# Performance work log

Measured on AMD Instinct MI355X. Metric: run time of the kernel, lower is better.

Reference implementation:

```python
import jax, jax.numpy as jnp
import numpy as np

N = 100_000      # nodes
E = 1_600_000    # edges (avg degree 16)
EP = 500_000     # pos/neg decode edges each
IN, H, OUT = 256, 128, 64


def setup_inputs() -> dict:
    key = jax.random.key(0)
    ks = jax.random.split(key, 8)
    x = jax.random.normal(ks[0], (N, IN), dtype=jnp.float32)
    edge_index = jax.random.randint(ks[1], (2, E), 0, N, dtype=jnp.int32)
    pos_edge_index = jax.random.randint(ks[2], (2, EP), 0, N, dtype=jnp.int32)
    neg_edge_index = jax.random.randint(ks[3], (2, EP), 0, N, dtype=jnp.int32)
    W1 = jax.random.normal(ks[4], (IN, H), dtype=jnp.float32) * (1.0 / np.sqrt(IN))
    b1 = jnp.zeros((H,), dtype=jnp.float32)
    W2 = jax.random.normal(ks[5], (H, OUT), dtype=jnp.float32) * (1.0 / np.sqrt(H))
    b2 = jnp.zeros((OUT,), dtype=jnp.float32)
    return dict(x=x, edge_index=edge_index, pos_edge_index=pos_edge_index,
                neg_edge_index=neg_edge_index, W1=W1, b1=b1, W2=W2, b2=b2)


def _gcn_conv(x, src, dst, norm, W, b, n_nodes):
    # PyG GCNConv: linear transform, then normalized scatter-add aggregation
    h = x @ W                              # [N, out]
    msg = h[src] * norm[:, None]           # gather + scale, [E+N, out]
    agg = jax.ops.segment_sum(msg, dst, num_segments=n_nodes)
    return agg + b


def reference(x, edge_index, pos_edge_index, neg_edge_index, W1, b1, W2, b2):
    n = x.shape[0]
    loops = jnp.arange(n, dtype=edge_index.dtype)
    src = jnp.concatenate([edge_index[0], loops])   # add self-loops (GCNConv default)
    dst = jnp.concatenate([edge_index[1], loops])
    # symmetric normalization D^{-1/2} (A+I) D^{-1/2}
    deg = jax.ops.segment_sum(jnp.ones_like(src, dtype=x.dtype), dst, num_segments=n)
    dinv = jnp.where(deg > 0, jax.lax.rsqrt(jnp.maximum(deg, 1e-12)), 0.0)
    norm = dinv[src] * dinv[dst]
    # encode
    h = jax.nn.relu(_gcn_conv(x, src, dst, norm, W1, b1, n))
    z = _gcn_conv(h, src, dst, norm, W2, b2, n)
    # decode: edge score = <z_u, z_v> over pos+neg edges
    ei = jnp.concatenate([pos_edge_index, neg_edge_index], axis=-1)
    return (z[ei[0]] * z[ei[1]]).sum(axis=-1)   # [2*EP]
```

## Files before the change

kernel.cpp:

```cpp
#include <hip/hip_runtime.h>


typedef __attribute__((ext_vector_type(8))) short short8;
typedef __attribute__((ext_vector_type(4))) float f32x4;

#define BUK_SHIFT 7
#define BUK_NODES 128

__global__ __launch_bounds__(256) void b_hist_k(const int* __restrict__ dst, int E,
                                                int nbuk, int* __restrict__ bhist) {
  __shared__ int h[1024];
  for (int i = threadIdx.x; i < nbuk; i += 256) h[i] = 0;
  __syncthreads();
  for (int i = blockIdx.x * 256 + threadIdx.x; i < E; i += gridDim.x * 256)
    atomicAdd(&h[dst[i] >> BUK_SHIFT], 1);
  __syncthreads();
  for (int i = threadIdx.x; i < nbuk; i += 256) {
    int c = h[i];
    if (c) atomicAdd(&bhist[i], c);
  }
}

__global__ __launch_bounds__(256) void b_scan_k(const int* __restrict__ bhist,
                                                int nbuk, int* __restrict__ bbase,
                                                int* __restrict__ bcur) {
  __shared__ int arr[256];
  const int t = threadIdx.x;
  const int per = (nbuk + 255) / 256;
  const int start = t * per;
  const int end = min(start + per, nbuk);
  int s = 0;
  for (int i = start; i < end; ++i) s += bhist[i];
  arr[t] = s;
  __syncthreads();
  for (int off = 1; off < 256; off <<= 1) {
    int v = (t >= off) ? arr[t - off] : 0;
    __syncthreads();
    arr[t] += v;
    __syncthreads();
  }
  int run = arr[t] - s;
  for (int i = start; i < end; ++i) {
    bbase[i] = run;
    bcur[i] = run;
    run += bhist[i];
  }
  if (t == 255) bbase[nbuk] = arr[255];
}

__global__ __launch_bounds__(256) void b_scatter_k(const int* __restrict__ src,
                                                   const int* __restrict__ dst, int E,
                                                   int nbuk, int* __restrict__ bcur,
                                                   int* __restrict__ ebuf) {
  __shared__ int lh[1024];
  __shared__ int lc[1024];
  const int base = blockIdx.x * 8192;
  if (base >= E) return;
  const int end = min(base + 8192, E);
  for (int i = threadIdx.x; i < nbuk; i += 256) lh[i] = 0;
  __syncthreads();
  for (int i = base + threadIdx.x; i < end; i += 256)
    atomicAdd(&lh[dst[i] >> BUK_SHIFT], 1);
  __syncthreads();
  for (int i = threadIdx.x; i < nbuk; i += 256) {
    int c = lh[i];
    lc[i] = c ? atomicAdd(&bcur[i], c) : 0;
  }
  __syncthreads();
  for (int i = base + threadIdx.x; i < end; i += 256) {
    int d = dst[i];
    int pos = atomicAdd(&lc[d >> BUK_SHIFT], 1);
    ebuf[pos] = src[i] | ((d & (BUK_NODES - 1)) << 17);
  }
}

__global__ __launch_bounds__(128) void b_build_k(const int* __restrict__ ebuf,
                                                 const int* __restrict__ bbase, int n,
                                                 int nbuk, float* __restrict__ dinv,
                                                 int* __restrict__ rowptr,
                                                 int* __restrict__ csr) {
  __shared__ int cnt[BUK_NODES];
  __shared__ int pre[BUK_NODES];
  __shared__ int cur[BUK_NODES];
  const int b = blockIdx.x, t = threadIdx.x;
  cnt[t] = 0;
  __syncthreads();
  const int beg = bbase[b], end = bbase[b + 1];
  for (int i = beg + t; i < end; i += 128) atomicAdd(&cnt[ebuf[i] >> 17], 1);
  __syncthreads();
  const int c = cnt[t];
  pre[t] = c;
  __syncthreads();
  for (int off = 1; off < 128; off <<= 1) {
    int v = (t >= off) ? pre[t - off] : 0;
    __syncthreads();
    pre[t] += v;
    __syncthreads();
  }
  const int base = beg + pre[t] - c;
  cur[t] = base;
  const int node = (b << BUK_SHIFT) + t;
  if (node < n) {
    rowptr[node] = base;
    dinv[node] = rsqrtf((float)(c + 1));
  }
  if (b == 0 && t == 0) rowptr[n] = bbase[nbuk];
  __syncthreads();
  for (int i = beg + t; i < end; i += 128) {
    int e = ebuf[i];
    int pos = atomicAdd(&cur[e >> 17], 1);
    csr[pos] = e & 0x1FFFF;
  }
}

__global__ __launch_bounds__(256) void split_w_k(const float* __restrict__ W, int K,
                                                 int N,
                                                 unsigned short* __restrict__ hi,
                                                 unsigned short* __restrict__ lo) {
  const int idx = blockIdx.x * 256 + threadIdx.x;
  if (idx >= K * N) return;
  const int k = idx / N, c = idx - k * N;
  const float a = W[idx];
  const unsigned u = __float_as_uint(a);
  const unsigned short h = (unsigned short)(u >> 16);
  const float l = a - __uint_as_float(u & 0xFFFF0000u);
  const unsigned short lb = (unsigned short)(__float_as_uint(l) >> 16);
  hi[(size_t)c * K + k] = h;
  lo[(size_t)c * K + k] = lb;
}

template <int BN>
__global__ __launch_bounds__(256) void gemm_mfma(
    const float* __restrict__ A, const unsigned short* __restrict__ Bthi,
    const unsigned short* __restrict__ Btlo, float* __restrict__ C,
    const float* __restrict__ rowscale, int M, int K) {
  constexpr int BM = 64, BK = 32;
  constexpr int NT = BN / 16;
  constexpr int LD = 40;
  __shared__ unsigned short Ahi[BM * LD];
  __shared__ unsigned short Alo[BM * LD];
  __shared__ unsigned short Bhi[BN * LD];
  __shared__ unsigned short Blo[BN * LD];
  const int tid = threadIdx.x;
  const int lane = tid & 63;
  const int wave = tid >> 6;
  const int rowBase = blockIdx.x * BM;

  f32x4 acc[NT];
#pragma unroll
  for (int c = 0; c < NT; ++c) acc[c] = (f32x4){0.f, 0.f, 0.f, 0.f};

  const int sr = tid >> 2;
  const int sk = (tid & 3) * 8;
  const int arow = wave * 16 + (lane & 15);
  const int akb = (lane >> 4) * 8;

  for (int k0 = 0; k0 < K; k0 += BK) {
    {
      const int gr = rowBase + sr;
      float4 v0 = make_float4(0.f, 0.f, 0.f, 0.f);
      float4 v1 = make_float4(0.f, 0.f, 0.f, 0.f);
      if (gr < M) {
        const float* p = A + (size_t)gr * K + k0 + sk;
        v0 = *reinterpret_cast<const float4*>(p);
        v1 = *reinterpret_cast<const float4*>(p + 4);
      }
      const float vv[8] = {v0.x, v0.y, v0.z, v0.w, v1.x, v1.y, v1.z, v1.w};
      short8 hv, lv;
#pragma unroll
      for (int i = 0; i < 8; ++i) {
        const unsigned u = __float_as_uint(vv[i]);
        hv[i] = (short)(u >> 16);
        const float l = vv[i] - __uint_as_float(u & 0xFFFF0000u);
        lv[i] = (short)(__float_as_uint(l) >> 16);
      }
      *reinterpret_cast<short8*>(&Ahi[sr * LD + sk]) = hv;
      *reinterpret_cast<short8*>(&Alo[sr * LD + sk]) = lv;
    }
    for (int i = tid; i < BN * 2; i += 256) {
      const int col = i >> 1;
      const int kk = (i & 1) * 16;
      const size_t gofs = (size_t)col * K + k0 + kk;
      *reinterpret_cast<short8*>(&Bhi[col * LD + kk]) =
          *reinterpret_cast<const short8*>(&Bthi[gofs]);
      *reinterpret_cast<short8*>(&Bhi[col * LD + kk + 8]) =
          *reinterpret_cast<const short8*>(&Bthi[gofs + 8]);
      *reinterpret_cast<short8*>(&Blo[col * LD + kk]) =
          *reinterpret_cast<const short8*>(&Btlo[gofs]);
      *reinterpret_cast<short8*>(&Blo[col * LD + kk + 8]) =
          *reinterpret_cast<const short8*>(&Btlo[gofs + 8]);
    }
    __syncthreads();
    const short8 fa_hi = *reinterpret_cast<const short8*>(&Ahi[arow * LD + akb]);
    const short8 fa_lo = *reinterpret_cast<const short8*>(&Alo[arow * LD + akb]);
#pragma unroll
    for (int c = 0; c < NT; ++c) {
      const int bofs = (c * 16 + (lane & 15)) * LD + akb;
      const short8 fb_hi = *reinterpret_cast<const short8*>(&Bhi[bofs]);
      const short8 fb_lo = *reinterpret_cast<const short8*>(&Blo[bofs]);
      acc[c] = __builtin_amdgcn_mfma_f32_16x16x32_bf16(fa_hi, fb_hi, acc[c], 0, 0, 0);
      acc[c] = __builtin_amdgcn_mfma_f32_16x16x32_bf16(fa_lo, fb_hi, acc[c], 0, 0, 0);
      acc[c] = __builtin_amdgcn_mfma_f32_16x16x32_bf16(fa_hi, fb_lo, acc[c], 0, 0, 0);
    }
    __syncthreads();
  }
  const int crow = rowBase + wave * 16 + (lane >> 4) * 4;
  float sc[4];
#pragma unroll
  for (int j = 0; j < 4; ++j) sc[j] = (crow + j < M) ? rowscale[crow + j] : 0.f;
#pragma unroll
  for (int c = 0; c < NT; ++c) {
#pragma unroll
    for (int j = 0; j < 4; ++j) {
      const int gr = crow + j;
      if (gr < M) C[(size_t)gr * BN + c * 16 + (lane & 15)] = acc[c][j] * sc[j];
    }
  }
}

template <bool RELU>
__global__ __launch_bounds__(256) void agg128_k(const float* __restrict__ g,
                                                const int* __restrict__ rowptr,
                                                const int* __restrict__ csr,
                                                const float* __restrict__ dinv,
                                                const float* __restrict__ bias,
                                                float* __restrict__ hout, int n) {
  const int wid = (blockIdx.x * 256 + threadIdx.x) >> 6;
  if (wid >= n) return;
  const int lane = threadIdx.x & 63;
  const int half = lane >> 5;
  const size_t col = (size_t)(lane & 31) * 4;
  const float dd = dinv[wid];
  const int beg = rowptr[wid];
  const int end = rowptr[wid + 1];
  float4 acc = make_float4(0.f, 0.f, 0.f, 0.f);
  int e = beg;
  for (; e + 8 <= end; e += 8) {
    const int s0 = csr[e + 0 + half];
    const int s1 = csr[e + 2 + half];
    const int s2 = csr[e + 4 + half];
    const int s3 = csr[e + 6 + half];
    const float4 v0 = *reinterpret_cast<const float4*>(&g[(size_t)s0 * 128 + col]);
    const float4 v1 = *reinterpret_cast<const float4*>(&g[(size_t)s1 * 128 + col]);
    const float4 v2 = *reinterpret_cast<const float4*>(&g[(size_t)s2 * 128 + col]);
    const float4 v3 = *reinterpret_cast<const float4*>(&g[(size_t)s3 * 128 + col]);
    acc.x += (v0.x + v1.x) + (v2.x + v3.x);
    acc.y += (v0.y + v1.y) + (v2.y + v3.y);
    acc.z += (v0.z + v1.z) + (v2.z + v3.z);
    acc.w += (v0.w + v1.w) + (v2.w + v3.w);
  }
  for (; e + 2 <= end; e += 2) {
    const int s = csr[e + half];
    const float4 v = *reinterpret_cast<const float4*>(&g[(size_t)s * 128 + col]);
    acc.x += v.x;
    acc.y += v.y;
    acc.z += v.z;
    acc.w += v.w;
  }
  if (e < end && half == 0) {
    const int s = csr[e];
    const float4 v = *reinterpret_cast<const float4*>(&g[(size_t)s * 128 + col]);
    acc.x += v.x;
    acc.y += v.y;
    acc.z += v.z;
    acc.w += v.w;
  }
  acc.x += __shfl_xor(acc.x, 32);
  acc.y += __shfl_xor(acc.y, 32);
  acc.z += __shfl_xor(acc.z, 32);
  acc.w += __shfl_xor(acc.w, 32);
  if (half == 0) {
    const float4 sv = *reinterpret_cast<const float4*>(&g[(size_t)wid * 128 + col]);
    const float4 b = *reinterpret_cast<const float4*>(&bias[col]);
    float4 r;
    r.x = dd * (acc.x + sv.x) + b.x;
    r.y = dd * (acc.y + sv.y) + b.y;
    r.z = dd * (acc.z + sv.z) + b.z;
    r.w = dd * (acc.w + sv.w) + b.w;
    if (RELU) {
      r.x = fmaxf(r.x, 0.f);
      r.y = fmaxf(r.y, 0.f);
      r.z = fmaxf(r.z, 0.f);
      r.w = fmaxf(r.w, 0.f);
    }
    *reinterpret_cast<float4*>(&hout[(size_t)wid * 128 + col]) = r;
  }
}

__global__ __launch_bounds__(256) void agg64_k(const float* __restrict__ g,
                                               const int* __restrict__ rowptr,
                                               const int* __restrict__ csr,
                                               const float* __restrict__ dinv,
                                               const float* __restrict__ bias,
                                               float* __restrict__ hout, int n) {
  const int wid = (blockIdx.x * 256 + threadIdx.x) >> 6;
  if (wid >= n) return;
  const int lane = threadIdx.x & 63;
  const int quad = lane >> 4;
  const size_t col = (size_t)(lane & 15) * 4;
  const float dd = dinv[wid];
  const int beg = rowptr[wid];
  const int end = rowptr[wid + 1];
  float4 acc = make_float4(0.f, 0.f, 0.f, 0.f);
  int e = beg;
  for (; e + 16 <= end; e += 16) {
    const int s0 = csr[e + 0 + quad];
    const int s1 = csr[e + 4 + quad];
    const int s2 = csr[e + 8 + quad];
    const int s3 = csr[e + 12 + quad];
    const float4 v0 = *reinterpret_cast<const float4*>(&g[(size_t)s0 * 64 + col]);
    const float4 v1 = *reinterpret_cast<const float4*>(&g[(size_t)s1 * 64 + col]);
    const float4 v2 = *reinterpret_cast<const float4*>(&g[(size_t)s2 * 64 + col]);
    const float4 v3 = *reinterpret_cast<const float4*>(&g[(size_t)s3 * 64 + col]);
    acc.x += (v0.x + v1.x) + (v2.x + v3.x);
    acc.y += (v0.y + v1.y) + (v2.y + v3.y);
    acc.z += (v0.z + v1.z) + (v2.z + v3.z);
    acc.w += (v0.w + v1.w) + (v2.w + v3.w);
  }
  for (; e + 4 <= end; e += 4) {
    const int s = csr[e + quad];
    const float4 v = *reinterpret_cast<const float4*>(&g[(size_t)s * 64 + col]);
    acc.x += v.x;
    acc.y += v.y;
    acc.z += v.z;
    acc.w += v.w;
  }
  const int r = end - e;
  if (quad < r) {
    const int s = csr[e + quad];
    const float4 v = *reinterpret_cast<const float4*>(&g[(size_t)s * 64 + col]);
    acc.x += v.x;
    acc.y += v.y;
    acc.z += v.z;
    acc.w += v.w;
  }
  acc.x += __shfl_xor(acc.x, 16);
  acc.y += __shfl_xor(acc.y, 16);
  acc.z += __shfl_xor(acc.z, 16);
  acc.w += __shfl_xor(acc.w, 16);
  acc.x += __shfl_xor(acc.x, 32);
  acc.y += __shfl_xor(acc.y, 32);
  acc.z += __shfl_xor(acc.z, 32);
  acc.w += __shfl_xor(acc.w, 32);
  if (quad == 0) {
    const float4 sv = *reinterpret_cast<const float4*>(&g[(size_t)wid * 64 + col]);
    const float4 b = *reinterpret_cast<const float4*>(&bias[col]);
    float4 res;
    res.x = dd * (acc.x + sv.x) + b.x;
    res.y = dd * (acc.y + sv.y) + b.y;
    res.z = dd * (acc.z + sv.z) + b.z;
    res.w = dd * (acc.w + sv.w) + b.w;
    *reinterpret_cast<float4*>(&hout[(size_t)wid * 64 + col]) = res;
  }
}

__global__ __launch_bounds__(256) void decode_k(const int* __restrict__ pos,
                                                const int* __restrict__ neg,
                                                const float* __restrict__ z,
                                                float* __restrict__ out, int EP) {
  const long long t = (long long)blockIdx.x * 256 + threadIdx.x;
  const long long e = t >> 3;
  const int lane = (int)(t & 7);
  if (e >= 2LL * EP) return;
  int u, v;
  if (e < EP) {
    u = pos[e];
    v = pos[EP + e];
  } else {
    u = neg[e - EP];
    v = neg[EP + (e - EP)];
  }
  const float* zu = &z[(size_t)u * 64 + lane * 8];
  const float* zv = &z[(size_t)v * 64 + lane * 8];
  const float4 a0 = *reinterpret_cast<const float4*>(zu);
  const float4 a1 = *reinterpret_cast<const float4*>(zu + 4);
  const float4 b0 = *reinterpret_cast<const float4*>(zv);
  const float4 b1 = *reinterpret_cast<const float4*>(zv + 4);
  float p = a0.x * b0.x + a0.y * b0.y + a0.z * b0.z + a0.w * b0.w +
            a1.x * b1.x + a1.y * b1.y + a1.z * b1.z + a1.w * b1.w;
#pragma unroll
  for (int off = 4; off > 0; off >>= 1) p += __shfl_down(p, off, 8);
  if (lane == 0) out[e] = p;
}


extern "C" void kernel_launch(void* const* d_in, const int* in_sizes, int n_in,
                              void* d_out, int out_size, void* d_ws, size_t ws_size,
                              hipStream_t stream) {
  const float* x = (const float*)d_in[0];
  const int* ei = (const int*)d_in[1];
  const int* pos = (const int*)d_in[2];
  const int* neg = (const int*)d_in[3];
  const float* W1 = (const float*)d_in[4];
  const float* b1 = (const float*)d_in[5];
  const float* W2 = (const float*)d_in[6];
  const float* b2 = (const float*)d_in[7];
  float* out = (float*)d_out;

  const int H = in_sizes[5];
  const int IN = in_sizes[4] / H;
  const int OUT = in_sizes[7];
  const int N = in_sizes[0] / IN;
  const int E = in_sizes[1] / 2;
  const int EP = in_sizes[2] / 2;

  char* ws = (char*)d_ws;
  size_t off = 0;
  auto carve = [&](size_t bytes) -> char* {
    char* p = ws + off;
    off += (bytes + 255) & ~(size_t)255;
    return p;
  };
  const int NBUK = (N + BUK_NODES - 1) >> BUK_SHIFT;

  float* dinvb = (float*)carve((size_t)N * 4);
  int* rowptr = (int*)carve((size_t)(N + 1) * 4);
  int* bhist = (int*)carve((size_t)NBUK * 4);
  int* bbase = (int*)carve((size_t)(NBUK + 1) * 4);
  int* bcur = (int*)carve((size_t)NBUK * 4);
  int* ebuf = (int*)carve((size_t)E * 4);
  int* csr = (int*)carve((size_t)E * 4);
  float* bufA = (float*)carve((size_t)N * H * 4);
  float* bufB = (float*)carve((size_t)N * H * 4);
  unsigned short* w1hi = (unsigned short*)carve((size_t)IN * H * 2);
  unsigned short* w1lo = (unsigned short*)carve((size_t)IN * H * 2);
  unsigned short* w2hi = (unsigned short*)carve((size_t)H * OUT * 2);
  unsigned short* w2lo = (unsigned short*)carve((size_t)H * OUT * 2);
  (void)ws_size;

  const int* srcp = ei;
  const int* dstp = ei + E;

  split_w_k<<<(IN * H + 255) / 256, 256, 0, stream>>>(W1, IN, H, w1hi, w1lo);
  split_w_k<<<(H * OUT + 255) / 256, 256, 0, stream>>>(W2, H, OUT, w2hi, w2lo);

  hipMemsetAsync(bhist, 0, (size_t)NBUK * 4, stream);
  b_hist_k<<<512, 256, 0, stream>>>(dstp, E, NBUK, bhist);
  b_scan_k<<<1, 256, 0, stream>>>(bhist, NBUK, bbase, bcur);
  b_scatter_k<<<(E + 8191) / 8192, 256, 0, stream>>>(srcp, dstp, E, NBUK, bcur, ebuf);
  b_build_k<<<NBUK, 128, 0, stream>>>(ebuf, bbase, N, NBUK, dinvb, rowptr, csr);

  gemm_mfma<128><<<(N + 63) / 64, 256, 0, stream>>>(x, w1hi, w1lo, bufA, dinvb, N, IN);
  agg128_k<true><<<(N + 3) / 4, 256, 0, stream>>>(bufA, rowptr, csr, dinvb, b1,
                                                  bufB, N);
  gemm_mfma<64><<<(N + 63) / 64, 256, 0, stream>>>(bufB, w2hi, w2lo, bufA, dinvb, N, H);
  agg64_k<<<(N + 3) / 4, 256, 0, stream>>>(bufA, rowptr, csr, dinvb, b2, bufB, N);
  const long long threads = 2LL * EP * 8;
  decode_k<<<(int)((threads + 255) / 256), 256, 0, stream>>>(pos, neg, bufB, out, EP);
}
```

Measured before the change: 377.7 us.

## Fuse layer-1 aggregation with layer-2 GEMM via shared-memory bf16 split tiles

Layer-1 neighbor aggregation (with bias and ReLU) now writes each 16-node tile into shared memory as hi/lo bf16 splits. The same block then multiplies the tile by W2 with MFMA and scales by dinv. This removes the global write and re-read of the 128-wide hidden activation and one kernel launch. In exchange, W2 fragments are loaded from global per block, and each block does a small MFMA tail after a barrier.

Measured after the change: 376.7 us. About the same (-0.3%).

```diff
diff --git a/kernel.cpp b/kernel.cpp
--- a/kernel.cpp
+++ b/kernel.cpp
@@ -218,72 +218,115 @@
   }
 }
 
-template <bool RELU>
-__global__ __launch_bounds__(256) void agg128_k(const float* __restrict__ g,
-                                                const int* __restrict__ rowptr,
-                                                const int* __restrict__ csr,
-                                                const float* __restrict__ dinv,
-                                                const float* __restrict__ bias,
-                                                float* __restrict__ hout, int n) {
-  const int wid = (blockIdx.x * 256 + threadIdx.x) >> 6;
-  if (wid >= n) return;
-  const int lane = threadIdx.x & 63;
+__global__ __launch_bounds__(256) void agg128_gemm2_k(
+    const float* __restrict__ g1, const int* __restrict__ rowptr,
+    const int* __restrict__ csr, const float* __restrict__ dinv,
+    const float* __restrict__ bias, const unsigned short* __restrict__ W2thi,
+    const unsigned short* __restrict__ W2tlo, float* __restrict__ g2, int n) {
+  constexpr int LD2 = 136;
+  __shared__ unsigned short Hhi[16 * LD2];
+  __shared__ unsigned short Hlo[16 * LD2];
+  const int tid = threadIdx.x;
+  const int lane = tid & 63;
+  const int wave = tid >> 6;
   const int half = lane >> 5;
+  const int nb = blockIdx.x * 16;
+
   const size_t col = (size_t)(lane & 31) * 4;
-  const float dd = dinv[wid];
-  const int beg = rowptr[wid];
-  const int end = rowptr[wid + 1];
-  float4 acc = make_float4(0.f, 0.f, 0.f, 0.f);
-  int e = beg;
-  for (; e + 8 <= end; e += 8) {
-    const int s0 = csr[e + 0 + half];
-    const int s1 = csr[e + 2 + half];
-    const int s2 = csr[e + 4 + half];
-    const int s3 = csr[e + 6 + half];
-    const float4 v0 = *reinterpret_cast<const float4*>(&g[(size_t)s0 * 128 + col]);
-    const float4 v1 = *reinterpret_cast<const float4*>(&g[(size_t)s1 * 128 + col]);
-    const float4 v2 = *reinterpret_cast<const float4*>(&g[(size_t)s2 * 128 + col]);
-    const float4 v3 = *reinterpret_cast<const float4*>(&g[(size_t)s3 * 128 + col]);
-    acc.x += (v0.x + v1.x) + (v2.x + v3.x);
-    acc.y += (v0.y + v1.y) + (v2.y + v3.y);
-    acc.z += (v0.z + v1.z) + (v2.z + v3.z);
-    acc.w += (v0.w + v1.w) + (v2.w + v3.w);
-  }
-  for (; e + 2 <= end; e += 2) {
-    const int s = csr[e + half];
-    const float4 v = *reinterpret_cast<const float4*>(&g[(size_t)s * 128 + col]);
-    acc.x += v.x;
-    acc.y += v.y;
-    acc.z += v.z;
-    acc.w += v.w;
-  }
-  if (e < end && half == 0) {
-    const int s = csr[e];
-    const float4 v = *reinterpret_cast<const float4*>(&g[(size_t)s * 128 + col]);
-    acc.x += v.x;
-    acc.y += v.y;
-    acc.z += v.z;
-    acc.w += v.w;
-  }
-  acc.x += __shfl_xor(acc.x, 32);
-  acc.y += __shfl_xor(acc.y, 32);
-  acc.z += __shfl_xor(acc.z, 32);
-  acc.w += __shfl_xor(acc.w, 32);
-  if (half == 0) {
-    const float4 sv = *reinterpret_cast<const float4*>(&g[(size_t)wid * 128 + col]);
-    const float4 b = *reinterpret_cast<const float4*>(&bias[col]);
-    float4 r;
-    r.x = dd * (acc.x + sv.x) + b.x;
-    r.y = dd * (acc.y + sv.y) + b.y;
-    r.z = dd * (acc.z + sv.z) + b.z;
-    r.w = dd * (acc.w + sv.w) + b.w;
-    if (RELU) {
-      r.x = fmaxf(r.x, 0.f);
-      r.y = fmaxf(r.y, 0.f);
-      r.z = fmaxf(r.z, 0.f);
-      r.w = fmaxf(r.w, 0.f);
-    }
-    *reinterpret_cast<float4*>(&hout[(size_t)wid * 128 + col]) = r;
+#pragma unroll
+  for (int it = 0; it < 4; ++it) {
+    const int row = wave * 4 + it;
+    const int node = nb + row;
+    float4 r = make_float4(0.f, 0.f, 0.f, 0.f);
+    if (node < n) {
+      const float dd = dinv[node];
+      const int beg = rowptr[node];
+      const int end = rowptr[node + 1];
+      float4 acc = make_float4(0.f, 0.f, 0.f, 0.f);
+      int e = beg;
+      for (; e + 8 <= end; e += 8) {
+        const int s0 = csr[e + 0 + half];
+        const int s1 = csr[e + 2 + half];
+        const int s2 = csr[e + 4 + half];
+        const int s3 = csr[e + 6 + half];
+        const float4 v0 = *reinterpret_cast<const float4*>(&g1[(size_t)s0 * 128 + col]);
+        const float4 v1 = *reinterpret_cast<const float4*>(&g1[(size_t)s1 * 128 + col]);
+        const float4 v2 = *reinterpret_cast<const float4*>(&g1[(size_t)s2 * 128 + col]);
+        const float4 v3 = *reinterpret_cast<const float4*>(&g1[(size_t)s3 * 128 + col]);
+        acc.x += (v0.x + v1.x) + (v2.x + v3.x);
+        acc.y += (v0.y + v1.y) + (v2.y + v3.y);
+        acc.z += (v0.z + v1.z) + (v2.z + v3.z);
+        acc.w += (v0.w + v1.w) + (v2.w + v3.w);
+      }
+      for (; e + 2 <= end; e += 2) {
+        const int s = csr[e + half];
+        const float4 v = *reinterpret_cast<const float4*>(&g1[(size_t)s * 128 + col]);
+        acc.x += v.x;
+        acc.y += v.y;
+        acc.z += v.z;
+        acc.w += v.w;
+      }
+      if (e < end && half == 0) {
+        const int s = csr[e];
+        const float4 v = *reinterpret_cast<const float4*>(&g1[(size_t)s * 128 + col]);
+        acc.x += v.x;
+        acc.y += v.y;
+        acc.z += v.z;
+        acc.w += v.w;
+      }
+      acc.x += __shfl_xor(acc.x, 32);
+      acc.y += __shfl_xor(acc.y, 32);
+      acc.z += __shfl_xor(acc.z, 32);
+      acc.w += __shfl_xor(acc.w, 32);
+      if (half == 0) {
+        const float4 sv = *reinterpret_cast<const float4*>(&g1[(size_t)node * 128 + col]);
+        const float4 b = *reinterpret_cast<const float4*>(&bias[col]);
+        r.x = fmaxf(dd * (acc.x + sv.x) + b.x, 0.f);
+        r.y = fmaxf(dd * (acc.y + sv.y) + b.y, 0.f);
+        r.z = fmaxf(dd * (acc.z + sv.z) + b.z, 0.f);
+        r.w = fmaxf(dd * (acc.w + sv.w) + b.w, 0.f);
+      }
+    }
+    if (half == 0) {
+      const float vv[4] = {r.x, r.y, r.z, r.w};
+      ushort4 hv, lv;
+      unsigned u0 = __float_as_uint(vv[0]);
+      unsigned u1 = __float_as_uint(vv[1]);
+      unsigned u2 = __float_as_uint(vv[2]);
+      unsigned u3 = __float_as_uint(vv[3]);
+      hv.x = (unsigned short)(u0 >> 16);
+      hv.y = (unsigned short)(u1 >> 16);
+      hv.z = (unsigned short)(u2 >> 16);
+      hv.w = (unsigned short)(u3 >> 16);
+      lv.x = (unsigned short)(__float_as_uint(vv[0] - __uint_as_float(u0 & 0xFFFF0000u)) >> 16);
+      lv.y = (unsigned short)(__float_as_uint(vv[1] - __uint_as_float(u1 & 0xFFFF0000u)) >> 16);
+      lv.z = (unsigned short)(__float_as_uint(vv[2] - __uint_as_float(u2 & 0xFFFF0000u)) >> 16);
+      lv.w = (unsigned short)(__float_as_uint(vv[3] - __uint_as_float(u3 & 0xFFFF0000u)) >> 16);
+      *reinterpret_cast<ushort4*>(&Hhi[row * LD2 + (lane & 31) * 4]) = hv;
+      *reinterpret_cast<ushort4*>(&Hlo[row * LD2 + (lane & 31) * 4]) = lv;
+    }
+  }
+  __syncthreads();
+
+  const int ct = wave * 16;
+  const int fr = lane & 15;
+  const int fk = (lane >> 4) * 8;
+  f32x4 acc2 = (f32x4){0.f, 0.f, 0.f, 0.f};
+#pragma unroll
+  for (int c = 0; c < 4; ++c) {
+    const short8 fa_hi = *reinterpret_cast<const short8*>(&Hhi[fr * LD2 + c * 32 + fk]);
+    const short8 fa_lo = *reinterpret_cast<const short8*>(&Hlo[fr * LD2 + c * 32 + fk]);
+    const size_t bo = (size_t)(ct + fr) * 128 + c * 32 + fk;
+    const short8 fb_hi = *reinterpret_cast<const short8*>(&W2thi[bo]);
+    const short8 fb_lo = *reinterpret_cast<const short8*>(&W2tlo[bo]);
+    acc2 = __builtin_amdgcn_mfma_f32_16x16x32_bf16(fa_hi, fb_hi, acc2, 0, 0, 0);
+    acc2 = __builtin_amdgcn_mfma_f32_16x16x32_bf16(fa_lo, fb_hi, acc2, 0, 0, 0);
+    acc2 = __builtin_amdgcn_mfma_f32_16x16x32_bf16(fa_hi, fb_lo, acc2, 0, 0, 0);
+  }
+#pragma unroll
+  for (int j = 0; j < 4; ++j) {
+    const int node = nb + (lane >> 4) * 4 + j;
+    if (node < n) g2[(size_t)node * 64 + ct + fr] = acc2[j] * dinv[node];
   }
 }
 
@@ -441,10 +484,9 @@
   b_build_k<<<NBUK, 128, 0, stream>>>(ebuf, bbase, N, NBUK, dinvb, rowptr, csr);
 
   gemm_mfma<128><<<(N + 63) / 64, 256, 0, stream>>>(x, w1hi, w1lo, bufA, dinvb, N, IN);
-  agg128_k<true><<<(N + 3) / 4, 256, 0, stream>>>(bufA, rowptr, csr, dinvb, b1,
-                                                  bufB, N);
-  gemm_mfma<64><<<(N + 63) / 64, 256, 0, stream>>>(bufB, w2hi, w2lo, bufA, dinvb, N, H);
-  agg64_k<<<(N + 3) / 4, 256, 0, stream>>>(bufA, rowptr, csr, dinvb, b2, bufB, N);
+  agg128_gemm2_k<<<(N + 15) / 16, 256, 0, stream>>>(bufA, rowptr, csr, dinvb, b1,
+                                                    w2hi, w2lo, bufB, N);
+  agg64_k<<<(N + 3) / 4, 256, 0, stream>>>(bufB, rowptr, csr, dinvb, b2, bufA, N);
   const long long threads = 2LL * EP * 8;
-  decode_k<<<(int)((threads + 255) / 256), 256, 0, stream>>>(pos, neg, bufB, out, EP);
-}
+  decode_k<<<(int)((threads + 255) / 256), 256, 0, stream>>>(pos, neg, bufA, out, EP);
+}
```
